# Performance work log

Measured on AMD Instinct MI355X. Metric: run time of the kernel, lower is better.

## Reference

```python
import jax, jax.numpy as jnp
import numpy as np

N_CLASSES = 64  # number of initial (labeled) classes


def _compute_logits_radii(h, protos, radii):
    """Complex-valued radii logits.
    h: [B,N,2,D] (real/imag), protos: [B,2,C,D], radii: [B,C].
    dist[b,n,c] = sum_d (hr-pr)^2 + (hi-pi)^2 (matches _compute_distances_complex).
    logits = -dist / (2*radii)  (standard IMP radii-logit form).
    Expanded as |h|^2 + |p|^2 - 2 h.p so the cross term is a GEMM (no [N,C,D] tensor).
    """
    hr, hi = h[:, :, 0, :], h[:, :, 1, :]          # [B,N,D]
    pr, pi = protos[:, 0], protos[:, 1]            # [B,C,D]
    h_sq = jnp.sum(hr * hr + hi * hi, axis=-1)     # [B,N]
    p_sq = jnp.sum(pr * pr + pi * pi, axis=-1)     # [B,C]
    cross = jnp.einsum('bnd,bcd->bnc', hr, pr) + jnp.einsum('bnd,bcd->bnc', hi, pi)
    dist = h_sq[:, :, None] + p_sq[:, None, :] - 2.0 * cross   # [B,N,C]
    return -dist / (2.0 * radii[:, None, :])


def setup_inputs() -> dict:
    key = jax.random.key(0)
    k1, k2, k3, k4, k5 = jax.random.split(key, 5)
    B, N, C, D = 1, 8192, 512, 512
    h = jax.random.normal(k1, (B, N, 2, D), dtype=jnp.float32)
    protos = jax.random.normal(k2, (B, 2, C, D), dtype=jnp.float32)
    # radii must be positive (it divides the distance); keep away from 0
    radii = jax.random.uniform(k3, (B, C), dtype=jnp.float32) * 0.9 + 0.1
    y = jax.random.randint(k4, (N,), 0, N_CLASSES)
    support_labels = jax.random.randint(k5, (C,), 0, N_CLASSES)
    return {"h": h, "protos": protos, "radii": radii, "y": y,
            "support_labels": support_labels, "n_initial_clusters": N_CLASSES}


def reference(h, protos, radii, y, support_labels, n_initial_clusters):
    logits = _compute_logits_radii(h, protos, radii)[0]          # [N,C], B=1 squeeze
    labels = jnp.where(y >= n_initial_clusters, -1, y)           # [N]
    support_targets = labels[:, None] == support_labels[None, :]  # [N,C] bool

    neg_inf = jnp.asarray(-jnp.inf, logits.dtype)
    # best prototype among the query's own class ('or' target)
    target_logits = jnp.where(support_targets, logits, neg_inf)
    best_targets = jnp.argmax(target_logits, axis=1)             # [N]

    # vectorized per-class best prototype: weights[n,c]=1 iff c is the argmax
    # of logits[n,:] restricted to clusters whose label == support_labels[c]
    max_per_class = jax.ops.segment_max(logits.T, support_labels,
                                        num_segments=N_CLASSES)  # [K,N]
    weights = (logits == max_per_class[support_labels, :].T).astype(logits.dtype)  # [N,C]

    # weighted cross entropy at the 'or' target
    log_probs = jax.nn.log_softmax(logits, axis=1)
    nll = -jnp.take_along_axis(log_probs, best_targets[:, None], axis=1)[:, 0]
    w = jnp.take_along_axis(weights, best_targets[:, None], axis=1)[:, 0]
    loss = jnp.mean(nll * w)

    # accuracy: predicted cluster -> its class label
    support_preds = jnp.argmax(logits, axis=1)
    y_pred = support_labels[support_preds]
    acc_val = jnp.sum((y_pred == labels).astype(jnp.float32))
    return loss, acc_val
```

## Files before the change

### kernel.cpp

```cpp
#include <hip/hip_runtime.h>
#include <stdint.h>

typedef unsigned short u16;
typedef __attribute__((ext_vector_type(8))) short shortx8;
typedef __attribute__((ext_vector_type(4))) float floatx4;

#define N_ROWS 8192
#define N_COLS 512
#define KDIM   1024

__device__ __forceinline__ u16 f2bf(float f) {
    union { float f; uint32_t u; } x; x.f = f;
    uint32_t u = x.u;
    uint32_t r = (u + 0x7FFFu + ((u >> 16) & 1u)) >> 16;
    return (u16)r;
}

__device__ __forceinline__ void async_copy16(const void* g, void* l) {
    __builtin_amdgcn_global_load_lds(
        (const __attribute__((address_space(1))) void*)g,
        (__attribute__((address_space(3))) void*)l, 16, 0, 0);
}

__global__ __launch_bounds__(256) void conv_hp(const float* __restrict__ h,
                                               const float* __restrict__ protos,
                                               u16* __restrict__ hb,
                                               u16* __restrict__ bb,
                                               float* __restrict__ hsq,
                                               float* __restrict__ psq,
                                               float* __restrict__ out) {
    int t = threadIdx.x, lane = t & 63, w = t >> 6;
    int bid = blockIdx.x;
    if (bid == 639 && t < 2) out[t] = 0.0f;
    if (bid < 512) {
        int wave = bid * 4 + w;
        for (int q = 0; q < 4; q++) {
            int row = wave * 4 + q;
            const float4* src = (const float4*)(h + (size_t)row * KDIM);
            ushort4* dst = (ushort4*)(hb + (size_t)row * KDIM);
            float s = 0.0f;
            #pragma unroll
            for (int j = 0; j < 4; j++) {
                float4 v = src[lane + j * 64];
                s += v.x * v.x + v.y * v.y + v.z * v.z + v.w * v.w;
                dst[lane + j * 64] = make_ushort4(f2bf(v.x), f2bf(v.y), f2bf(v.z), f2bf(v.w));
            }
            #pragma unroll
            for (int off = 32; off; off >>= 1) s += __shfl_xor(s, off);
            if (lane == 0) hsq[row] = s;
        }
    } else {
        int c = (bid - 512) * 4 + w;
        const float4* pr = (const float4*)(protos + (size_t)c * 512);
        const float4* pi = (const float4*)(protos + 512 * 512 + (size_t)c * 512);
        ushort4* dr = (ushort4*)(bb + (size_t)c * KDIM);
        ushort4* di = (ushort4*)(bb + (size_t)c * KDIM + 512);
        float s = 0.0f;
        #pragma unroll
        for (int j = 0; j < 2; j++) {
            float4 a = pr[lane + j * 64];
            float4 b = pi[lane + j * 64];
            s += a.x * a.x + a.y * a.y + a.z * a.z + a.w * a.w;
            s += b.x * b.x + b.y * b.y + b.z * b.z + b.w * b.w;
            dr[lane + j * 64] = make_ushort4(f2bf(a.x), f2bf(a.y), f2bf(a.z), f2bf(a.w));
            di[lane + j * 64] = make_ushort4(f2bf(b.x), f2bf(b.y), f2bf(b.z), f2bf(b.w));
        }
        #pragma unroll
        for (int off = 32; off; off >>= 1) s += __shfl_xor(s, off);
        if (lane == 0) psq[c] = s;
    }
}

__global__ __launch_bounds__(256) void gemm_partials(const u16* __restrict__ hb,
                                                     const u16* __restrict__ bb,
                                                     const float* __restrict__ hsq,
                                                     const float* __restrict__ psq,
                                                     const float* __restrict__ radii,
                                                     const int* __restrict__ y,
                                                     const int* __restrict__ slab,
                                                     const int* __restrict__ ninit_p,
                                                     float* __restrict__ pmax_g,
                                                     int* __restrict__ pidx_g,
                                                     float* __restrict__ prmax_g,
                                                     float* __restrict__ pc0_g,
                                                     float* __restrict__ psum_g,
                                                     float* __restrict__ l0arr) {
    constexpr int BM = 128, BN = 64, BK = 64;
    __shared__ __align__(16) u16 As[2][BM * BK];
    __shared__ __align__(16) u16 Bs[2][BN * BK];
    __shared__ float smax[2][128];
    __shared__ int   scol[2][128];
    __shared__ float srmx[2][128];
    __shared__ float sc0v[2][128];
    __shared__ float ssum[2][128];

    int t = threadIdx.x, lane = t & 63, w = t >> 6;
    int wr = (w & 1) * 64;
    int wc = (w >> 1) * 32;
    int bm0 = blockIdx.x * BM;
    int bn0 = blockIdx.y * BN;

    int tr = t >> 3, tc = t & 7;
    const u16* gA[4]; int loA[4];
    #pragma unroll
    for (int i = 0; i < 4; i++) {
        int row = tr + 32 * i;
        int kc = tc ^ (row & 7);
        gA[i] = hb + (size_t)(bm0 + row) * KDIM + kc * 8;
        loA[i] = (t + 256 * i) * 8;
    }
    const u16* gB[2]; int loB[2];
    #pragma unroll
    for (int i = 0; i < 2; i++) {
        int row = tr + 32 * i;
        int kc = tc ^ (row & 7);
        gB[i] = bb + (size_t)(bn0 + row) * KDIM + kc * 8;
        loB[i] = (t + 256 * i) * 8;
    }

    floatx4 acc[4][2] = {};

    int kq = lane >> 4, l7 = lane & 7, m = lane & 15;
    int swz0 = ((kq) ^ l7) * 8;
    int swz1 = ((4 + kq) ^ l7) * 8;

    #pragma unroll
    for (int i = 0; i < 4; i++) { async_copy16(gA[i], &As[0][loA[i]]); gA[i] += BK; }
    #pragma unroll
    for (int i = 0; i < 2; i++) { async_copy16(gB[i], &Bs[0][loB[i]]); gB[i] += BK; }

    int buf = 0;
    for (int k0 = 0; k0 < KDIM; k0 += BK) {
        __syncthreads();
        if (k0 + BK < KDIM) {
            int nb = buf ^ 1;
            #pragma unroll
            for (int i = 0; i < 4; i++) { async_copy16(gA[i], &As[nb][loA[i]]); gA[i] += BK; }
            #pragma unroll
            for (int i = 0; i < 2; i++) { async_copy16(gB[i], &Bs[nb][loB[i]]); gB[i] += BK; }
        }
        const u16* paA = &As[buf][(wr + m) * BK];
        const u16* paB = &Bs[buf][(wc + m) * BK];
        #pragma unroll
        for (int s = 0; s < 2; s++) {
            int sw = s ? swz1 : swz0;
            shortx8 af[4], bf[2];
            #pragma unroll
            for (int i = 0; i < 4; i++) af[i] = *(const shortx8*)(paA + i * 16 * BK + sw);
            #pragma unroll
            for (int j = 0; j < 2; j++) bf[j] = *(const shortx8*)(paB + j * 16 * BK + sw);
            #pragma unroll
            for (int i = 0; i < 4; i++)
                #pragma unroll
                for (int j = 0; j < 2; j++)
                    acc[i][j] = __builtin_amdgcn_mfma_f32_16x16x32_bf16(af[i], bf[j], acc[i][j], 0, 0, 0);
        }
        buf ^= 1;
    }

    int c0 = bn0 + wc + m, c1 = c0 + 16;
    float ps0 = psq[c0], ps1 = psq[c1];
    float inv0 = 0.5f / radii[c0], inv1 = 0.5f / radii[c1];
    int sl0 = slab[c0], sl1 = slab[c1];
    int slabz = slab[0];
    int ninit = ninit_p[0];
    int ch = w >> 1;
    bool isL0 = (bn0 == 0) && (wc == 0) && (m == 0);

    #pragma unroll
    for (int i = 0; i < 4; i++) {
        #pragma unroll
        for (int r = 0; r < 4; r++) {
            int n = bm0 + wr + i * 16 + kq * 4 + r;
            float hsqn = hsq[n];
            int yv = y[n];
            int lab = (yv >= ninit) ? -1 : yv;
            float v0 = (2.0f * acc[i][0][r] - hsqn - ps0) * inv0;
            float v1 = (2.0f * acc[i][1][r] - hsqn - ps1) * inv1;
            if (isL0) l0arr[n] = v0;

            float bmax = v0; int bcol = c0;
            if (v1 > bmax) { bmax = v1; bcol = c1; }
            float brm = -INFINITY;
            if (sl0 == lab) brm = v0;
            if (sl1 == lab && v1 > brm) brm = v1;
            float bc0 = -INFINITY;
            if (sl0 == slabz) bc0 = v0;
            if (sl1 == slabz && v1 > bc0) bc0 = v1;
            #pragma unroll
            for (int off = 1; off < 16; off <<= 1) {
                float ov = __shfl_xor(bmax, off); int oc = __shfl_xor(bcol, off);
                if (ov > bmax || (ov == bmax && oc < bcol)) { bmax = ov; bcol = oc; }
                float orv = __shfl_xor(brm, off); if (orv > brm) brm = orv;
                float oc0 = __shfl_xor(bc0, off); if (oc0 > bc0) bc0 = oc0;
            }
            float se = __expf(v0 - bmax) + __expf(v1 - bmax);
            #pragma unroll
            for (int off = 1; off < 16; off <<= 1) se += __shfl_xor(se, off);
            if (m == 0) {
                int rl = (w & 1) * 64 + i * 16 + kq * 4 + r;
                smax[ch][rl] = bmax; scol[ch][rl] = bcol;
                srmx[ch][rl] = brm;  sc0v[ch][rl] = bc0; ssum[ch][rl] = se;
            }
        }
    }
    __syncthreads();
    if (t < 128) {
        int n = bm0 + t;
        size_t gi_ = (size_t)blockIdx.y * N_ROWS + n;
        float m0 = smax[0][t], m1 = smax[1][t];
        int i0 = scol[0][t], i1 = scol[1][t];
        float gm; int gi;
        if (m0 > m1 || (m0 == m1 && i0 < i1)) { gm = m0; gi = i0; }
        else { gm = m1; gi = i1; }
        pmax_g[gi_] = gm;
        pidx_g[gi_] = gi;
        prmax_g[gi_] = fmaxf(srmx[0][t], srmx[1][t]);
        pc0_g[gi_]  = fmaxf(sc0v[0][t], sc0v[1][t]);
        psum_g[gi_] = ssum[0][t] * __expf(m0 - gm) + ssum[1][t] * __expf(m1 - gm);
    }
}

__global__ __launch_bounds__(256) void combine(const float* __restrict__ pmax_g,
                                               const int* __restrict__ pidx_g,
                                               const float* __restrict__ prmax_g,
                                               const float* __restrict__ pc0_g,
                                               const float* __restrict__ psum_g,
                                               const float* __restrict__ l0arr,
                                               const int* __restrict__ y,
                                               const int* __restrict__ slab,
                                               const int* __restrict__ ninit_p,
                                               float* __restrict__ out) {
    int t = threadIdx.x, lane = t & 63, w = t >> 6;
    int n = blockIdx.x * 256 + t;

    float gm = -INFINITY; int gi = 0x7fffffff;
    float rm = -INFINITY, c0m = -INFINITY;
    float pm[8];
    #pragma unroll
    for (int cb = 0; cb < 8; cb++) {
        size_t idx = (size_t)cb * N_ROWS + n;
        float p = pmax_g[idx]; int pi = pidx_g[idx];
        pm[cb] = p;
        if (p > gm || (p == gm && pi < gi)) { gm = p; gi = pi; }
        rm = fmaxf(rm, prmax_g[idx]);
        c0m = fmaxf(c0m, pc0_g[idx]);
    }
    float den = 0.0f;
    #pragma unroll
    for (int cb = 0; cb < 8; cb++)
        den += psum_g[(size_t)cb * N_ROWS + n] * __expf(pm[cb] - gm);
    float lse = gm + __logf(den);

    int yv = y[n];
    int lab = (yv >= ninit_p[0]) ? -1 : yv;
    float nll, wgt;
    if (rm != -INFINITY) { nll = lse - rm; wgt = 1.0f; }
    else {
        float l0 = l0arr[n];
        nll = lse - l0;
        wgt = (l0 == c0m) ? 1.0f : 0.0f;
    }
    int ypred = slab[gi];
    float li = nll * wgt * (1.0f / (float)N_ROWS);
    float ai = (ypred == lab) ? 1.0f : 0.0f;

    #pragma unroll
    for (int off = 32; off; off >>= 1) {
        li += __shfl_xor(li, off);
        ai += __shfl_xor(ai, off);
    }
    __shared__ float pl[4], pa_[4];
    if (lane == 0) { pl[w] = li; pa_[w] = ai; }
    __syncthreads();
    if (t == 0) {
        atomicAdd(&out[0], pl[0] + pl[1] + pl[2] + pl[3]);
        atomicAdd(&out[1], pa_[0] + pa_[1] + pa_[2] + pa_[3]);
    }
}

extern "C" void kernel_launch(void* const* d_in, const int* in_sizes, int n_in,
                              void* d_out, int out_size, void* d_ws, size_t ws_size,
                              hipStream_t stream) {
    const float* h      = (const float*)d_in[0];
    const float* protos = (const float*)d_in[1];
    const float* radii  = (const float*)d_in[2];
    const int*   y      = (const int*)d_in[3];
    const int*   slab   = (const int*)d_in[4];
    const int*   ninit  = (const int*)d_in[5];
    float* out = (float*)d_out;

    char* ws = (char*)d_ws;
    u16*   hb    = (u16*)(ws);
    u16*   bb    = (u16*)(ws + 16777216);
    float* hsq   = (float*)(ws + 17825792);
    float* psq   = (float*)(ws + 17858560);
    float* pmax  = (float*)(ws + 17860608);
    int*   pidx  = (int*)  (ws + 18122752);
    float* prmax = (float*)(ws + 18384896);
    float* pc0   = (float*)(ws + 18647040);
    float* psum  = (float*)(ws + 18909184);
    float* l0arr = (float*)(ws + 19171328);

    conv_hp<<<640, 256, 0, stream>>>(h, protos, hb, bb, hsq, psq, out);
    dim3 g(N_ROWS / 128, N_COLS / 64);
    gemm_partials<<<g, 256, 0, stream>>>(hb, bb, hsq, psq, radii, y, slab, ninit,
                                         pmax, pidx, prmax, pc0, psum, l0arr);
    combine<<<N_ROWS / 256, 256, 0, stream>>>(pmax, pidx, prmax, pc0, psum,
                                              l0arr, y, slab, ninit, out);
}
```

Before: 119.0 us.

## Load GEMM MFMA fragments directly from global memory, dropping LDS staging

Removes the double-buffered LDS staging (async global-to-LDS copies, swizzled shared tiles, per-K-step barriers) from the bf16 GEMM. Each wave now reads its MFMA operand fragments straight from global memory with 16-byte loads in an unrolled K loop. This removes barrier and LDS traffic, but each block's A and B tiles are now fetched separately by the waves that share them, so redundant reads are left to the caches and the loads are less coalesced (16 bytes per lane across rows).

```diff
diff --git a/kernel.cpp b/kernel.cpp
--- a/kernel.cpp
+++ b/kernel.cpp
@@ -14,12 +14,6 @@
     uint32_t u = x.u;
     uint32_t r = (u + 0x7FFFu + ((u >> 16) & 1u)) >> 16;
     return (u16)r;
-}
-
-__device__ __forceinline__ void async_copy16(const void* g, void* l) {
-    __builtin_amdgcn_global_load_lds(
-        (const __attribute__((address_space(1))) void*)g,
-        (__attribute__((address_space(3))) void*)l, 16, 0, 0);
 }
 
 __global__ __launch_bounds__(256) void conv_hp(const float* __restrict__ h,
@@ -85,9 +79,7 @@
                                                      float* __restrict__ pc0_g,
                                                      float* __restrict__ psum_g,
                                                      float* __restrict__ l0arr) {
-    constexpr int BM = 128, BN = 64, BK = 64;
-    __shared__ __align__(16) u16 As[2][BM * BK];
-    __shared__ __align__(16) u16 Bs[2][BN * BK];
+    constexpr int BM = 128, BN = 64;
     __shared__ float smax[2][128];
     __shared__ int   scol[2][128];
     __shared__ float srmx[2][128];
@@ -100,62 +92,31 @@
     int bm0 = blockIdx.x * BM;
     int bn0 = blockIdx.y * BN;
 
-    int tr = t >> 3, tc = t & 7;
-    const u16* gA[4]; int loA[4];
-    #pragma unroll
-    for (int i = 0; i < 4; i++) {
-        int row = tr + 32 * i;
-        int kc = tc ^ (row & 7);
-        gA[i] = hb + (size_t)(bm0 + row) * KDIM + kc * 8;
-        loA[i] = (t + 256 * i) * 8;
-    }
-    const u16* gB[2]; int loB[2];
-    #pragma unroll
-    for (int i = 0; i < 2; i++) {
-        int row = tr + 32 * i;
-        int kc = tc ^ (row & 7);
-        gB[i] = bb + (size_t)(bn0 + row) * KDIM + kc * 8;
-        loB[i] = (t + 256 * i) * 8;
-    }
+    int m = lane & 15, kq = lane >> 4;
+
+    const u16* pA[4]; const u16* pB[2];
+    #pragma unroll
+    for (int i = 0; i < 4; i++)
+        pA[i] = hb + (size_t)(bm0 + wr + i * 16 + m) * KDIM + kq * 8;
+    #pragma unroll
+    for (int j = 0; j < 2; j++)
+        pB[j] = bb + (size_t)(bn0 + wc + j * 16 + m) * KDIM + kq * 8;
 
     floatx4 acc[4][2] = {};
 
-    int kq = lane >> 4, l7 = lane & 7, m = lane & 15;
-    int swz0 = ((kq) ^ l7) * 8;
-    int swz1 = ((4 + kq) ^ l7) * 8;
-
-    #pragma unroll
-    for (int i = 0; i < 4; i++) { async_copy16(gA[i], &As[0][loA[i]]); gA[i] += BK; }
-    #pragma unroll
-    for (int i = 0; i < 2; i++) { async_copy16(gB[i], &Bs[0][loB[i]]); gB[i] += BK; }
-
-    int buf = 0;
-    for (int k0 = 0; k0 < KDIM; k0 += BK) {
-        __syncthreads();
-        if (k0 + BK < KDIM) {
-            int nb = buf ^ 1;
-            #pragma unroll
-            for (int i = 0; i < 4; i++) { async_copy16(gA[i], &As[nb][loA[i]]); gA[i] += BK; }
-            #pragma unroll
-            for (int i = 0; i < 2; i++) { async_copy16(gB[i], &Bs[nb][loB[i]]); gB[i] += BK; }
-        }
-        const u16* paA = &As[buf][(wr + m) * BK];
-        const u16* paB = &Bs[buf][(wc + m) * BK];
-        #pragma unroll
-        for (int s = 0; s < 2; s++) {
-            int sw = s ? swz1 : swz0;
-            shortx8 af[4], bf[2];
-            #pragma unroll
-            for (int i = 0; i < 4; i++) af[i] = *(const shortx8*)(paA + i * 16 * BK + sw);
-            #pragma unroll
-            for (int j = 0; j < 2; j++) bf[j] = *(const shortx8*)(paB + j * 16 * BK + sw);
-            #pragma unroll
-            for (int i = 0; i < 4; i++)
-                #pragma unroll
-                for (int j = 0; j < 2; j++)
-                    acc[i][j] = __builtin_amdgcn_mfma_f32_16x16x32_bf16(af[i], bf[j], acc[i][j], 0, 0, 0);
-        }
-        buf ^= 1;
+    #pragma unroll 8
+    for (int ks = 0; ks < KDIM / 32; ks++) {
+        int ko = ks * 32;
+        shortx8 af[4], bf[2];
+        #pragma unroll
+        for (int i = 0; i < 4; i++) af[i] = *(const shortx8*)(pA[i] + ko);
+        #pragma unroll
+        for (int j = 0; j < 2; j++) bf[j] = *(const shortx8*)(pB[j] + ko);
+        #pragma unroll
+        for (int i = 0; i < 4; i++)
+            #pragma unroll
+            for (int j = 0; j < 2; j++)
+                acc[i][j] = __builtin_amdgcn_mfma_f32_16x16x32_bf16(af[i], bf[j], acc[i][j], 0, 0, 0);
     }
 
     int c0 = bn0 + wc + m, c1 = c0 + 16;
```

New measurement: 147.8 us. +24.2%, slower.
